# Kernel optimization log

Measured on AMD Instinct MI355X. Metric: run time of the kernel, lower is better.

Reference implementation:

```python
import jax, jax.numpy as jnp
import numpy as np

# dims
B, S, D, H = 16, 2048, 512, 512  # batch, seq, input_size, hidden


def _qrnn_dir(X, W, b):
    """Single-direction QRNN (window=1, output gate, fo-pooling).
    X: [S, B, Din]; W: [Din, 3H]; b: [3H]. Returns [S, B, H]."""
    ZFO = jnp.einsum('sbd,dh->sbh', X, W) + b
    Z, F, O = jnp.split(ZFO, 3, axis=-1)
    Z = jnp.tanh(Z)
    F = jax.nn.sigmoid(F)
    O = jax.nn.sigmoid(O)

    def step(c, zf):
        z, f = zf
        c = f * c + (1.0 - f) * z
        return c, c

    c0 = jnp.zeros(Z.shape[1:], Z.dtype)
    _, C = jax.lax.scan(step, c0, (Z, F))
    return O * C


def _bi_layer(X, Wf, bf, Wb, bb):
    Yf = _qrnn_dir(X, Wf, bf)
    Yb = _qrnn_dir(X[::-1], Wb, bb)[::-1]
    return jnp.concatenate([Yf, Yb], axis=2)


def setup_inputs() -> dict:
    key = jax.random.key(0)
    ks = jax.random.split(key, 10)
    X = jax.random.normal(ks[0], (B, S, D), dtype=jnp.float32)
    seqlens = jax.random.randint(ks[1], (B,), 1, S + 1)

    def lin(k, din):
        kw, kb = jax.random.split(k)
        W = jax.random.normal(kw, (din, 3 * H), dtype=jnp.float32) * (1.0 / np.sqrt(din))
        bb_ = jax.random.normal(kb, (3 * H,), dtype=jnp.float32) * 0.01
        return W, bb_

    W_fw0, b_fw0 = lin(ks[2], D)
    W_bw0, b_bw0 = lin(ks[3], D)
    W_fw1, b_fw1 = lin(ks[4], 2 * H)
    W_bw1, b_bw1 = lin(ks[5], 2 * H)
    return {
        'X': X, 'seqlens': seqlens,
        'W_fw0': W_fw0, 'b_fw0': b_fw0, 'W_bw0': W_bw0, 'b_bw0': b_bw0,
        'W_fw1': W_fw1, 'b_fw1': b_fw1, 'W_bw1': W_bw1, 'b_bw1': b_bw1,
    }


def reference(X, seqlens, W_fw0, b_fw0, W_bw0, b_bw0, W_fw1, b_fw1, W_bw1, b_bw1):
    # batch_first -> time-major (seq, batch, feat); seqlens is unused (as in original)
    Xt = jnp.transpose(X, (1, 0, 2))
    Y1 = _bi_layer(Xt, W_fw0, b_fw0, W_bw0, b_bw0)  # [S, B, 2H]
    Y2 = _bi_layer(Y1, W_fw1, b_fw1, W_bw1, b_bw1)  # [S, B, 2H]
    return jnp.transpose(Y2, (1, 0, 2))  # [B, S, 2H]
```

## Files before the change

### kernel.cpp

```cpp
#include <hip/hip_runtime.h>
#include <hip/hip_fp16.h>
#include <math.h>
#include <stdint.h>
#include <type_traits>

#define SQ   2048
#define HID  512
#define N3   1536
#define N2   1024
#define NB   16
#define NC   64
#define NCLOG 6
#define LCH  32

#define BM 256
#define BN 256
#define BK 64

typedef __attribute__((ext_vector_type(8))) _Float16 half8;
typedef __attribute__((ext_vector_type(4))) _Float16 half4v;
typedef __attribute__((ext_vector_type(2))) _Float16 half2v;
typedef __attribute__((ext_vector_type(4))) float    floatx4;
typedef __attribute__((ext_vector_type(2))) float    floatx2;

__device__ __forceinline__ void load16_lds(const void* g, void* l) {
    __builtin_amdgcn_global_load_lds(
        (const __attribute__((address_space(1))) uint32_t*)g,
        (__attribute__((address_space(3))) uint32_t*)l, 16, 0, 0);
}

__device__ __forceinline__ float fast_sigmoid(float v) {
    return __builtin_amdgcn_rcpf(1.0f + __expf(-v));
}
__device__ __forceinline__ float fast_tanh(float v) {
    return 1.0f - 2.0f * __builtin_amdgcn_rcpf(1.0f + __expf(2.0f * v));
}

__global__ __launch_bounds__(256) void convert_fp16(
    const float* __restrict__ X, _Float16* __restrict__ Xh, long n)
{
    long i = ((long)blockIdx.x * 256 + threadIdx.x) * 4;
    if (i < n) {
        floatx4 v = *(const floatx4*)(X + i);
        half4v h = { (_Float16)v[0], (_Float16)v[1], (_Float16)v[2], (_Float16)v[3] };
        *(half4v*)(Xh + i) = h;
    }
}

__global__ __launch_bounds__(256) void transpose_w(
    const float* __restrict__ W, _Float16* __restrict__ Wt, int K)
{
    __shared__ float t[32][33];
    int k0 = blockIdx.x * 32, n0 = blockIdx.y * 32;
    int x  = threadIdx.x & 31;
    int y4 = (threadIdx.x >> 5) * 4;
    #pragma unroll
    for (int i = 0; i < 4; ++i)
        t[y4 + i][x] = W[(size_t)(k0 + y4 + i) * N3 + n0 + x];
    __syncthreads();
    #pragma unroll
    for (int i = 0; i < 4; ++i)
        Wt[(size_t)(n0 + y4 + i) * K + k0 + x] = (_Float16)t[x][y4 + i];
}

#define LOAD_A(LA, KK, IH) do { _Pragma("unroll") \
    for (int i = 0; i < 4; ++i) { \
        int row = wm * 128 + ((IH) * 4 + i) * 16 + m16; \
        af[i] = *(const half8*)&(LA)[row * 64 + (((KK) * 4 + kb) ^ (row & 7)) * 8]; \
    } } while (0)

#define LOAD_B(LB, KK) do { _Pragma("unroll") \
    for (int j = 0; j < 4; ++j) { \
        int row = wn * 64 + j * 16 + m16; \
        bf[j] = *(const half8*)&(LB)[row * 64 + (((KK) * 4 + kb) ^ (row & 7)) * 8]; \
    } } while (0)

#define MFMA16(IH) do { _Pragma("unroll") \
    for (int i = 0; i < 4; ++i) { _Pragma("unroll") \
        for (int j = 0; j < 4; ++j) \
            acc[(IH) * 4 + i][j] = __builtin_amdgcn_mfma_f32_16x16x32_f16( \
                af[i], bf[j], acc[(IH) * 4 + i][j], 0, 0, 0); \
    } } while (0)

#define STAGE_HALF(GB, ROW0, T, LDST) do { \
    const _Float16* _g = (GB) + (size_t)((ROW0) + w8s) * K + (size_t)(T) * BK + sch8; \
    load16_lds(_g, (LDST) + w * 512); \
    load16_lds(_g + (size_t)64 * K, (LDST) + 4096 + w * 512); \
} while (0)

#define VM2 asm volatile("s_waitcnt vmcnt(2)" ::: "memory")
#define VM0 asm volatile("s_waitcnt vmcnt(0)" ::: "memory")

#define PHASE(CBUF, KK, IH, STAGES, VMC) do { \
    LOAD_A(&lds[CBUF][0][0], KK, IH); \
    if ((IH) == 0) LOAD_B(&lds[CBUF][1][0], KK); \
    STAGES; \
    VMC; \
    __builtin_amdgcn_s_barrier(); \
    asm volatile("s_waitcnt lgkmcnt(0)" ::: "memory"); \
    __builtin_amdgcn_sched_barrier(0); \
    __builtin_amdgcn_s_setprio(1); \
    MFMA16(IH); \
    __builtin_amdgcn_s_setprio(0); \
    __builtin_amdgcn_sched_barrier(0); \
    __builtin_amdgcn_s_barrier(); \
} while (0)

__global__ __launch_bounds__(512, 2) void qrnn_gemm_bias_act(
    const _Float16* __restrict__ A,
    const _Float16* __restrict__ Wt,
    const float* __restrict__ bias,
    _Float16* __restrict__ ZOh,
    float* __restrict__ Ff,
    int K)
{
    __shared__ _Float16 lds[2][2][BM * BK];

    const int nwg  = gridDim.x;
    const int cpx  = nwg >> 3;
    const int orig = blockIdx.x;
    const int lin  = (orig & 7) * cpx + (orig >> 3);
    const int NT   = N3 / BN;
    const int ntile = lin % NT;
    const int mtile = lin / NT;
    const int m0 = mtile * BM;
    const int n0 = ntile * BN;

    const int tid  = threadIdx.x;
    const int lane = tid & 63;
    const int w    = tid >> 6;
    const int wm   = w >> 2;
    const int wn   = w & 3;
    const int m16  = lane & 15;
    const int kb   = lane >> 4;

    const int srow = lane >> 3;
    const int sch8 = ((lane & 7) ^ srow) * 8;
    const int w8s  = w * 8 + srow;

    const _Float16* gAb = A  + (size_t)m0 * K;
    const _Float16* gBb = Wt + (size_t)n0 * K;

    floatx4 acc[8][4] = {};
    half8 af[4], bf[4];

    const int nt = K / BK;
    const int ni = nt / 2;

    STAGE_HALF(gAb, 0,   0, &lds[0][0][0]);
    STAGE_HALF(gAb, 128, 0, &lds[0][0][8192]);
    STAGE_HALF(gBb, 0,   0, &lds[0][1][0]);
    STAGE_HALF(gBb, 128, 0, &lds[0][1][8192]);
    STAGE_HALF(gBb, 0,   1, &lds[1][1][0]);
    VM2;
    __builtin_amdgcn_s_barrier();
    __builtin_amdgcn_sched_barrier(0);

    for (int it = 0; it < ni - 1; ++it) {
        const int t1 = 2 * it + 1;
        const int t2 = 2 * it + 2;
        const int t3 = 2 * it + 3;

        PHASE(0, 0, 0, { STAGE_HALF(gAb, 0,   t1, &lds[1][0][0]);    }, );
        PHASE(0, 0, 1, { STAGE_HALF(gAb, 128, t1, &lds[1][0][8192]); }, );
        PHASE(0, 1, 0, { STAGE_HALF(gBb, 128, t1, &lds[1][1][8192]); }, );
        PHASE(0, 1, 1, { STAGE_HALF(gBb, 0,   t2, &lds[0][1][0]);    }, VM2);
        PHASE(1, 0, 0, { STAGE_HALF(gAb, 0,   t2, &lds[0][0][0]);    }, );
        PHASE(1, 0, 1, { STAGE_HALF(gAb, 128, t2, &lds[0][0][8192]); }, );
        PHASE(1, 1, 0, { STAGE_HALF(gBb, 128, t2, &lds[0][1][8192]); }, );
        PHASE(1, 1, 1, { STAGE_HALF(gBb, 0,   t3, &lds[1][1][0]);    }, VM2);
    }

    {
        const int t1 = nt - 1;
        PHASE(0, 0, 0, { STAGE_HALF(gAb, 0,   t1, &lds[1][0][0]);    }, );
        PHASE(0, 0, 1, { STAGE_HALF(gAb, 128, t1, &lds[1][0][8192]); }, );
        PHASE(0, 1, 0, { STAGE_HALF(gBb, 128, t1, &lds[1][1][8192]); }, );
        PHASE(0, 1, 1, { }, VM0);
        PHASE(1, 0, 0, { }, );
        PHASE(1, 0, 1, { }, );
        PHASE(1, 1, 0, { }, );
        PHASE(1, 1, 1, { }, );
    }

    const int rbase = (lane >> 4) * 4;
    const int cbase = lane & 15;
    const int rtype = (n0 >= 2 * HID) ? 2 : ((n0 >= HID) ? 1 : 0);
    float bvj[4];
    #pragma unroll
    for (int j = 0; j < 4; ++j)
        bvj[j] = bias[n0 + wn * 64 + j * 16 + cbase];

    if (rtype == 0) {
        #pragma unroll
        for (int i = 0; i < 8; ++i)
            #pragma unroll
            for (int j = 0; j < 4; ++j) {
                int n = n0 + wn * 64 + j * 16 + cbase;
                #pragma unroll
                for (int r = 0; r < 4; ++r) {
                    int m = m0 + wm * 128 + i * 16 + rbase + r;
                    ZOh[(size_t)m * N2 + n] =
                        (_Float16)fast_tanh(acc[i][j][r] + bvj[j]);
                }
            }
    } else if (rtype == 1) {
        #pragma unroll
        for (int i = 0; i < 8; ++i)
            #pragma unroll
            for (int j = 0; j < 4; ++j) {
                int n = n0 + wn * 64 + j * 16 + cbase;
                #pragma unroll
                for (int r = 0; r < 4; ++r) {
                    int m = m0 + wm * 128 + i * 16 + rbase + r;
                    Ff[(size_t)m * HID + (n - HID)] =
                        fast_sigmoid(acc[i][j][r] + bvj[j]);
                }
            }
    } else {
        #pragma unroll
        for (int i = 0; i < 8; ++i)
            #pragma unroll
            for (int j = 0; j < 4; ++j) {
                int n = n0 + wn * 64 + j * 16 + cbase;
                #pragma unroll
                for (int r = 0; r < 4; ++r) {
                    int m = m0 + wm * 128 + i * 16 + rbase + r;
                    ZOh[(size_t)m * N2 + (n - HID)] =
                        (_Float16)fast_sigmoid(acc[i][j][r] + bvj[j]);
                }
            }
    }
}


__global__ __launch_bounds__(256) void qrnn_scan_sum(
    const _Float16* __restrict__ ZOh, const float* __restrict__ Ff,
    floatx2* __restrict__ Fs, floatx2* __restrict__ Cs,
    int reverse)
{
    int t  = blockIdx.x * 256 + threadIdx.x;
    int hh = t & 255;
    int bj = t >> 8;
    int j  = bj & (NC - 1);
    int b  = bj >> NCLOG;
    int h2 = hh * 2;
    const _Float16* zb = ZOh + (size_t)b * SQ * N2 + h2;
    const float*    fb = Ff  + (size_t)b * SQ * HID + h2;
    float F0 = 1.f, F1 = 1.f, c0 = 0.f, c1 = 0.f;
    int s0 = j * LCH;
    #pragma unroll 4
    for (int i = 0; i < LCH; ++i) {
        int s = reverse ? (s0 + LCH - 1 - i) : (s0 + i);
        half2v zh  = *(const half2v*)(zb + (size_t)s * N2);
        floatx2 f  = *(const floatx2*)(fb + (size_t)s * HID);
        F0 *= f[0]; F1 *= f[1];
        c0 = f[0] * c0 + (1.f - f[0]) * (float)zh[0];
        c1 = f[1] * c1 + (1.f - f[1]) * (float)zh[1];
    }
    Fs[(size_t)bj * 256 + hh] = floatx2{F0, F1};
    Cs[(size_t)bj * 256 + hh] = floatx2{c0, c1};
}

__global__ __launch_bounds__(256) void qrnn_scan_mid(
    const floatx2* __restrict__ Fs, const floatx2* __restrict__ Cs,
    floatx2* __restrict__ cin, int reverse)
{
    int t  = blockIdx.x * 256 + threadIdx.x;
    int hh = t & 255;
    int b  = t >> 8;
    float c0 = 0.f, c1 = 0.f;
    for (int i = 0; i < NC; ++i) {
        int j = reverse ? (NC - 1 - i) : i;
        size_t idx = ((size_t)b * NC + j) * 256 + hh;
        cin[idx] = floatx2{c0, c1};
        floatx2 F = Fs[idx], C = Cs[idx];
        c0 = F[0] * c0 + C[0];
        c1 = F[1] * c1 + C[1];
    }
}

template <typename OT>
__global__ __launch_bounds__(256) void qrnn_scan_out(
    const _Float16* __restrict__ ZOh, const float* __restrict__ Ff,
    const floatx2* __restrict__ cin,
    OT* __restrict__ out,
    int reverse, int col_ofs)
{
    int t  = blockIdx.x * 256 + threadIdx.x;
    int hh = t & 255;
    int bj = t >> 8;
    int j  = bj & (NC - 1);
    int b  = bj >> NCLOG;
    int h2 = hh * 2;
    const _Float16* zb = ZOh + (size_t)b * SQ * N2 + h2;
    const float*    fb = Ff  + (size_t)b * SQ * HID + h2;
    floatx2 c = cin[(size_t)bj * 256 + hh];
    float c0 = c[0], c1 = c[1];
    int s0 = j * LCH;
    #pragma unroll 4
    for (int i = 0; i < LCH; ++i) {
        int s = reverse ? (s0 + LCH - 1 - i) : (s0 + i);
        half2v zh  = *(const half2v*)(zb + (size_t)s * N2);
        half2v oh  = *(const half2v*)(zb + (size_t)s * N2 + HID);
        floatx2 f  = *(const floatx2*)(fb + (size_t)s * HID);
        c0 = f[0] * c0 + (1.f - f[0]) * (float)zh[0];
        c1 = f[1] * c1 + (1.f - f[1]) * (float)zh[1];
        OT* q = out + (size_t)(b * SQ + s) * N2 + col_ofs + h2;
        if constexpr (std::is_same<OT, float>::value) {
            *(floatx2*)q = floatx2{(float)oh[0] * c0, (float)oh[1] * c1};
        } else {
            *(half2v*)q = half2v{(_Float16)((float)oh[0] * c0),
                                 (_Float16)((float)oh[1] * c1)};
        }
    }
}

extern "C" void kernel_launch(void* const* d_in, const int* in_sizes, int n_in,
                              void* d_out, int out_size, void* d_ws, size_t ws_size,
                              hipStream_t stream)
{
    const float* X = (const float*)d_in[0];
    const float* Wd[2][2] = {
        { (const float*)d_in[2], (const float*)d_in[4] },
        { (const float*)d_in[6], (const float*)d_in[8] } };
    const float* bd[2][2] = {
        { (const float*)d_in[3], (const float*)d_in[5] },
        { (const float*)d_in[7], (const float*)d_in[9] } };
    float* OUT = (float*)d_out;

    char* p = (char*)d_ws;
    _Float16* Y1 = (_Float16*)p;  p += (size_t)NB * SQ * N2 * sizeof(_Float16);
    _Float16* Xh = (_Float16*)p;  p += (size_t)NB * SQ * 512 * sizeof(_Float16);
    _Float16* Wt = (_Float16*)p;  p += (size_t)N3 * 1024 * sizeof(_Float16);
    size_t sum_elems = (size_t)NB * NC * 256;
    floatx2* Fs  = (floatx2*)p;   p += sum_elems * sizeof(floatx2);
    floatx2* Cs  = (floatx2*)p;   p += sum_elems * sizeof(floatx2);
    floatx2* cin = (floatx2*)p;   p += sum_elems * sizeof(floatx2);
    size_t used  = (size_t)(p - (char*)d_ws);
    size_t per_b = (size_t)SQ * (N2 * sizeof(_Float16) + HID * sizeof(float));
    size_t avail = (ws_size > used) ? (ws_size - used) : per_b;
    int cbmax = (int)(avail / per_b);
    if (cbmax > NB) cbmax = NB;
    if (cbmax < 1)  cbmax = 1;
    _Float16* ZOh = (_Float16*)p;
    float*    Ff  = (float*)(p + (size_t)cbmax * SQ * N2 * sizeof(_Float16));

    {
        long n = (long)NB * SQ * 512;
        convert_fp16<<<(int)(n / 4 / 256), 256, 0, stream>>>(X, Xh, n);
    }

    for (int layer = 0; layer < 2; ++layer) {
        int K = (layer == 0) ? 512 : 1024;
        const _Float16* Ah = (layer == 0) ? Xh : Y1;
        for (int dir = 0; dir < 2; ++dir) {
            transpose_w<<<dim3(K / 32, N3 / 32), 256, 0, stream>>>(
                Wd[layer][dir], Wt, K);
            int colofs = (dir == 0) ? 0 : HID;
            for (int c0 = 0; c0 < NB; c0 += cbmax) {
                int cb = (cbmax < NB - c0) ? cbmax : (NB - c0);
                int M = cb * SQ;
                int nwg = (M / BM) * (N3 / BN);
                qrnn_gemm_bias_act<<<dim3(nwg), 512, 0, stream>>>(
                    Ah + (size_t)c0 * SQ * K, Wt, bd[layer][dir], ZOh, Ff, K);
                qrnn_scan_sum<<<cb * NC, 256, 0, stream>>>(ZOh, Ff, Fs, Cs, dir);
                qrnn_scan_mid<<<cb, 256, 0, stream>>>(Fs, Cs, cin, dir);
                if (layer == 0) {
                    qrnn_scan_out<_Float16><<<cb * NC, 256, 0, stream>>>(
                        ZOh, Ff, cin, Y1 + (size_t)c0 * SQ * N2, dir, colofs);
                } else {
                    qrnn_scan_out<float><<<cb * NC, 256, 0, stream>>>(
                        ZOh, Ff, cin, OUT + (size_t)c0 * SQ * N2, dir, colofs);
                }
            }
        }
    }
}
```

Before: 749.4 us.

## Restructure GEMM main loop into 4-stage BK=32 pipeline with register double-buffering

After: 961.2 us. 28.3% more time.

```diff
diff --git a/kernel.cpp b/kernel.cpp
--- a/kernel.cpp
+++ b/kernel.cpp
@@ -15,7 +15,7 @@
 
 #define BM 256
 #define BN 256
-#define BK 64
+#define BK 32
 
 typedef __attribute__((ext_vector_type(8))) _Float16 half8;
 typedef __attribute__((ext_vector_type(4))) _Float16 half4v;
@@ -63,47 +63,38 @@
         Wt[(size_t)(n0 + y4 + i) * K + k0 + x] = (_Float16)t[x][y4 + i];
 }
 
-#define LOAD_A(LA, KK, IH) do { _Pragma("unroll") \
-    for (int i = 0; i < 4; ++i) { \
-        int row = wm * 128 + ((IH) * 4 + i) * 16 + m16; \
-        af[i] = *(const half8*)&(LA)[row * 64 + (((KK) * 4 + kb) ^ (row & 7)) * 8]; \
-    } } while (0)
-
-#define LOAD_B(LB, KK) do { _Pragma("unroll") \
-    for (int j = 0; j < 4; ++j) { \
-        int row = wn * 64 + j * 16 + m16; \
-        bf[j] = *(const half8*)&(LB)[row * 64 + (((KK) * 4 + kb) ^ (row & 7)) * 8]; \
-    } } while (0)
-
-#define MFMA16(IH) do { _Pragma("unroll") \
-    for (int i = 0; i < 4; ++i) { _Pragma("unroll") \
+#define VM8 asm volatile("s_waitcnt vmcnt(8)" ::: "memory")
+#define VM4 asm volatile("s_waitcnt vmcnt(4)" ::: "memory")
+#define VM0 asm volatile("s_waitcnt vmcnt(0)" ::: "memory")
+#define BARSYNC do { __builtin_amdgcn_s_barrier(); \
+                     __builtin_amdgcn_sched_barrier(0); } while (0)
+
+#define STAGE_T(T, BUF) do { \
+    const long _to = (long)(T) * BK; \
+    load16_lds(gA0 + _to, &lds[BUF][0][w * 512]); \
+    load16_lds(gA1 + _to, &lds[BUF][0][4096 + w * 512]); \
+    load16_lds(gB0 + _to, &lds[BUF][1][w * 512]); \
+    load16_lds(gB1 + _to, &lds[BUF][1][4096 + w * 512]); \
+} while (0)
+
+#define READS_T(BUF, AF, BF) do { _Pragma("unroll") \
+    for (int i = 0; i < 8; ++i) \
+        AF[i] = *(const half8*)&lds[BUF][0][(wm * 128 + i * 16 + m16) * BK + sl8]; \
+    _Pragma("unroll") \
+    for (int j = 0; j < 4; ++j) \
+        BF[j] = *(const half8*)&lds[BUF][1][(wn * 64 + j * 16 + m16) * BK + sl8]; \
+} while (0)
+
+#define MFMA_T(AF, BF) do { \
+    __builtin_amdgcn_s_setprio(1); \
+    _Pragma("unroll") \
+    for (int i = 0; i < 8; ++i) { _Pragma("unroll") \
         for (int j = 0; j < 4; ++j) \
-            acc[(IH) * 4 + i][j] = __builtin_amdgcn_mfma_f32_16x16x32_f16( \
-                af[i], bf[j], acc[(IH) * 4 + i][j], 0, 0, 0); \
-    } } while (0)
-
-#define STAGE_HALF(GB, ROW0, T, LDST) do { \
-    const _Float16* _g = (GB) + (size_t)((ROW0) + w8s) * K + (size_t)(T) * BK + sch8; \
-    load16_lds(_g, (LDST) + w * 512); \
-    load16_lds(_g + (size_t)64 * K, (LDST) + 4096 + w * 512); \
-} while (0)
-
-#define VM2 asm volatile("s_waitcnt vmcnt(2)" ::: "memory")
-#define VM0 asm volatile("s_waitcnt vmcnt(0)" ::: "memory")
-
-#define PHASE(CBUF, KK, IH, STAGES, VMC) do { \
-    LOAD_A(&lds[CBUF][0][0], KK, IH); \
-    if ((IH) == 0) LOAD_B(&lds[CBUF][1][0], KK); \
-    STAGES; \
-    VMC; \
-    __builtin_amdgcn_s_barrier(); \
-    asm volatile("s_waitcnt lgkmcnt(0)" ::: "memory"); \
-    __builtin_amdgcn_sched_barrier(0); \
-    __builtin_amdgcn_s_setprio(1); \
-    MFMA16(IH); \
+            acc[i][j] = __builtin_amdgcn_mfma_f32_16x16x32_f16( \
+                AF[i], BF[j], acc[i][j], 0, 0, 0); \
+    } \
     __builtin_amdgcn_s_setprio(0); \
     __builtin_amdgcn_sched_barrier(0); \
-    __builtin_amdgcn_s_barrier(); \
 } while (0)
 
 __global__ __launch_bounds__(512, 2) void qrnn_gemm_bias_act(
@@ -114,7 +105,7 @@
     float* __restrict__ Ff,
     int K)
 {
-    __shared__ _Float16 lds[2][2][BM * BK];
+    __shared__ _Float16 lds[4][2][BM * BK];
 
     const int nwg  = gridDim.x;
     const int cpx  = nwg >> 3;
@@ -133,55 +124,34 @@
     const int wn   = w & 3;
     const int m16  = lane & 15;
     const int kb   = lane >> 4;
-
-    const int srow = lane >> 3;
-    const int sch8 = ((lane & 7) ^ srow) * 8;
-    const int w8s  = w * 8 + srow;
-
-    const _Float16* gAb = A  + (size_t)m0 * K;
-    const _Float16* gBb = Wt + (size_t)n0 * K;
+    const int sl8  = kb * 8;
+
+    const _Float16* gA0 = A  + (size_t)(m0 + (tid >> 2)) * K + (tid & 3) * 8;
+    const _Float16* gA1 = gA0 + (size_t)128 * K;
+    const _Float16* gB0 = Wt + (size_t)(n0 + (tid >> 2)) * K + (tid & 3) * 8;
+    const _Float16* gB1 = gB0 + (size_t)128 * K;
 
     floatx4 acc[8][4] = {};
-    half8 af[4], bf[4];
+    half8 af0[8], bf0[4], af1[8], bf1[4];
 
     const int nt = K / BK;
-    const int ni = nt / 2;
-
-    STAGE_HALF(gAb, 0,   0, &lds[0][0][0]);
-    STAGE_HALF(gAb, 128, 0, &lds[0][0][8192]);
-    STAGE_HALF(gBb, 0,   0, &lds[0][1][0]);
-    STAGE_HALF(gBb, 128, 0, &lds[0][1][8192]);
-    STAGE_HALF(gBb, 0,   1, &lds[1][1][0]);
-    VM2;
-    __builtin_amdgcn_s_barrier();
-    __builtin_amdgcn_sched_barrier(0);
-
-    for (int it = 0; it < ni - 1; ++it) {
-        const int t1 = 2 * it + 1;
-        const int t2 = 2 * it + 2;
-        const int t3 = 2 * it + 3;
-
-        PHASE(0, 0, 0, { STAGE_HALF(gAb, 0,   t1, &lds[1][0][0]);    }, );
-        PHASE(0, 0, 1, { STAGE_HALF(gAb, 128, t1, &lds[1][0][8192]); }, );
-        PHASE(0, 1, 0, { STAGE_HALF(gBb, 128, t1, &lds[1][1][8192]); }, );
-        PHASE(0, 1, 1, { STAGE_HALF(gBb, 0,   t2, &lds[0][1][0]);    }, VM2);
-        PHASE(1, 0, 0, { STAGE_HALF(gAb, 0,   t2, &lds[0][0][0]);    }, );
-        PHASE(1, 0, 1, { STAGE_HALF(gAb, 128, t2, &lds[0][0][8192]); }, );
-        PHASE(1, 1, 0, { STAGE_HALF(gBb, 128, t2, &lds[0][1][8192]); }, );
-        PHASE(1, 1, 1, { STAGE_HALF(gBb, 0,   t3, &lds[1][1][0]);    }, VM2);
-    }
-
-    {
-        const int t1 = nt - 1;
-        PHASE(0, 0, 0, { STAGE_HALF(gAb, 0,   t1, &lds[1][0][0]);    }, );
-        PHASE(0, 0, 1, { STAGE_HALF(gAb, 128, t1, &lds[1][0][8192]); }, );
-        PHASE(0, 1, 0, { STAGE_HALF(gBb, 128, t1, &lds[1][1][8192]); }, );
-        PHASE(0, 1, 1, { }, VM0);
-        PHASE(1, 0, 0, { }, );
-        PHASE(1, 0, 1, { }, );
-        PHASE(1, 1, 0, { }, );
-        PHASE(1, 1, 1, { }, );
-    }
+
+    STAGE_T(0, 0); STAGE_T(1, 1); STAGE_T(2, 2);
+    VM8;
+    BARSYNC;
+    READS_T(0, af0, bf0);
+
+    for (int tb = 0; tb < nt - 4; tb += 4) {
+        STAGE_T(tb + 3, 3); VM8; BARSYNC; READS_T(1, af1, bf1); MFMA_T(af0, bf0);
+        STAGE_T(tb + 4, 0); VM8; BARSYNC; READS_T(2, af0, bf0); MFMA_T(af1, bf1);
+        STAGE_T(tb + 5, 1); VM8; BARSYNC; READS_T(3, af1, bf1); MFMA_T(af0, bf0);
+        STAGE_T(tb + 6, 2); VM8; BARSYNC; READS_T(0, af0, bf0); MFMA_T(af1, bf1);
+    }
+
+    STAGE_T(nt - 1, 3); VM8; BARSYNC; READS_T(1, af1, bf1); MFMA_T(af0, bf0);
+    VM4; BARSYNC; READS_T(2, af0, bf0); MFMA_T(af1, bf1);
+    VM0; BARSYNC; READS_T(3, af1, bf1); MFMA_T(af0, bf0);
+    VM0; BARSYNC;                         MFMA_T(af1, bf1);
 
     const int rbase = (lane >> 4) * 4;
     const int cbase = lane & 15;
```
